# Performance work log

Hardware: AMD Instinct MI355X
Metric: run time of the kernel (lower is better)

The kernel has to match this reference:

```python
import jax, jax.numpy as jnp
import numpy as np

EPS = 1e-8


def setup_inputs() -> dict:
    key = jax.random.key(0)
    ks = jax.random.split(key, 7)
    B, H, S, D = 4, 16, 4096, 64
    query = jax.random.normal(ks[0], (B, H, S, D), dtype=jnp.float32)
    k_in = jax.random.normal(ks[1], (B, H, S, D), dtype=jnp.float32)
    value = jax.random.normal(ks[2], (B, H, S, D), dtype=jnp.float32)
    output = jax.random.normal(ks[3], (B, H, S, D), dtype=jnp.float32)
    betas = jax.random.normal(ks[4], (H, 1, D), dtype=jnp.float32)
    init_states = jax.random.normal(ks[5], (H, D, D), dtype=jnp.float32)
    init_z = jax.random.uniform(ks[6], (H, D), dtype=jnp.float32)
    return {"query": query, "key": k_in, "value": value, "output": output,
            "betas": betas, "init_states": init_states, "init_z": init_z}


def reference(query, key, value, output, betas, init_states, init_z):
    # ---- compute updates (delta rule) ----
    sigma_k = jax.nn.elu(key) + 1.0                       # [B,H,S,D]
    # retrieved_value = (sigma_k @ states) / (sigma_k @ z + eps)
    num = jnp.einsum('bhsd,hde->bhse', sigma_k, init_states)   # [B,H,S,D]
    den = jnp.einsum('bhsd,hd->bhs', sigma_k, init_z)[..., None] + EPS
    value_update = value - num / den                      # delta rule
    # memory_states = init_states + sigma_k^T @ value_update -> [B,H,D,D]
    memory_states = init_states[None] + jnp.einsum('bhsd,bhse->bhde', sigma_k, value_update)
    memory_z = init_z[None] + sigma_k.sum(axis=-2)        # [B,H,D]
    # ---- retrieve memory ----
    sigma_q = jax.nn.elu(query) + 1.0                     # [B,H,S,D]
    retrieved = jnp.einsum('bhsd,bhde->bhse', sigma_q, memory_states)
    norm = jnp.einsum('bhsd,bhd->bhs', sigma_q, memory_z)[..., None] + EPS
    memory_output = retrieved / norm                      # [B,H,S,D]
    # ---- sigmoid-gated blend ----
    gate = jax.nn.sigmoid(betas)                          # [H,1,D] broadcasts over B,S
    return gate * memory_output + (1.0 - gate) * output
```

## Files before the change

### kernel.cpp

```cpp
#include <hip/hip_runtime.h>
#include <hip/hip_bf16.h>


#define B_  4
#define H_  16
#define S_  4096
#define D_  64
#define BH_ 64
#define EPS_ 1e-8f

typedef __attribute__((ext_vector_type(8))) short bf16x8;
typedef __attribute__((ext_vector_type(4))) float f32x4;

__device__ __forceinline__ unsigned short f2bf(float x) {
    union { float f; unsigned u; } v; v.f = x;
    return (unsigned short)((v.u + 0x7FFFu + ((v.u >> 16) & 1u)) >> 16);
}
__device__ __forceinline__ float elup1(float x) {
    return x > 0.0f ? x + 1.0f : __expf(x);
}
__device__ __forceinline__ f32x4 fzero() { f32x4 z = {0.f, 0.f, 0.f, 0.f}; return z; }

__global__ __launch_bounds__(256, 2) void k1_states(
    const float* __restrict__ Kp, const float* __restrict__ Vp,
    const float* __restrict__ W0, const float* __restrict__ Z0,
    float* __restrict__ Mpart, float* __restrict__ Zpart, int NS)
{
    const int bh = blockIdx.x / NS;
    const int p  = blockIdx.x % NS;
    const int h  = bh & (H_ - 1);
    const int tid  = threadIdx.x;
    const int lane = tid & 63;
    const int wave = tid >> 6;
    const int c16  = lane & 15;
    const int g4   = lane >> 4;

    __shared__ __align__(16) unsigned short skT[4][64][40];
    __shared__ __align__(16) unsigned short vuT[4][64][40];
    __shared__ float Mlds[64 * 65];
    __shared__ float Zlds[4][64];

    float z0v[2][8];
    #pragma unroll
    for (int kk = 0; kk < 2; ++kk) {
        f32x4 a = *(const f32x4*)(Z0 + h * 64 + kk * 32 + g4 * 8);
        f32x4 b = *(const f32x4*)(Z0 + h * 64 + kk * 32 + g4 * 8 + 4);
        #pragma unroll
        for (int j = 0; j < 4; ++j) { z0v[kk][j] = a[j]; z0v[kk][4 + j] = b[j]; }
    }

    bf16x8 w0f[4][2];
    #pragma unroll
    for (int et = 0; et < 4; ++et)
    #pragma unroll
    for (int kk = 0; kk < 2; ++kk) {
        bf16x8 f;
        #pragma unroll
        for (int j = 0; j < 8; ++j) {
            int d = kk * 32 + g4 * 8 + j;
            f[j] = (short)f2bf(W0[(size_t)h * 4096 + d * 64 + et * 16 + c16]);
        }
        w0f[et][kk] = f;
    }

    const size_t baseKV  = (size_t)bh * S_ * D_;
    const int    schunk  = S_ / NS;
    const int    ngroups = schunk / 32;

    f32x4 mpa[4][4];
    #pragma unroll
    for (int i = 0; i < 4; ++i)
    #pragma unroll
    for (int j = 0; j < 4; ++j) mpa[i][j] = fzero();
    float zacc[2][8];
    #pragma unroll
    for (int kk = 0; kk < 2; ++kk)
    #pragma unroll
    for (int j = 0; j < 8; ++j) zacc[kk][j] = 0.f;

    for (int g = wave; g < ngroups; g += 4) {
        const int row0 = p * schunk + g * 32;

        float sk[2][2][8];
        #pragma unroll
        for (int st = 0; st < 2; ++st) {
            const float* kr = Kp + baseKV + (size_t)(row0 + st * 16 + c16) * D_;
            #pragma unroll
            for (int kk = 0; kk < 2; ++kk) {
                f32x4 a = *(const f32x4*)(kr + kk * 32 + g4 * 8);
                f32x4 b = *(const f32x4*)(kr + kk * 32 + g4 * 8 + 4);
                #pragma unroll
                for (int j = 0; j < 4; ++j) {
                    sk[st][kk][j]     = elup1(a[j]);
                    sk[st][kk][4 + j] = elup1(b[j]);
                }
            }
        }

        float den0 = 0.f, den1 = 0.f;
        #pragma unroll
        for (int kk = 0; kk < 2; ++kk)
        #pragma unroll
        for (int j = 0; j < 8; ++j) {
            den0 += sk[0][kk][j] * z0v[kk][j];
            den1 += sk[1][kk][j] * z0v[kk][j];
        }
        den0 += __shfl_xor(den0, 16); den0 += __shfl_xor(den0, 32);
        den1 += __shfl_xor(den1, 16); den1 += __shfl_xor(den1, 32);
        const float rd0 = __builtin_amdgcn_rcpf(den0 + EPS_);
        const float rd1 = __builtin_amdgcn_rcpf(den1 + EPS_);

        #pragma unroll
        for (int kk = 0; kk < 2; ++kk)
        #pragma unroll
        for (int j = 0; j < 8; ++j) zacc[kk][j] += sk[0][kk][j] + sk[1][kk][j];

        bf16x8 skf[2][2];
        #pragma unroll
        for (int kk = 0; kk < 2; ++kk)
        #pragma unroll
        for (int j = 0; j < 8; ++j) {
            unsigned short b0 = f2bf(sk[0][kk][j]);
            unsigned short b1 = f2bf(sk[1][kk][j]);
            skf[0][kk][j] = (short)b0;
            skf[1][kk][j] = (short)b1;
            *(unsigned*)&skT[wave][kk * 32 + g4 * 8 + j][2 * c16] =
                (unsigned)b0 | ((unsigned)b1 << 16);
        }

        f32x4 acc[2][4];
        #pragma unroll
        for (int st = 0; st < 2; ++st)
        #pragma unroll
        for (int et = 0; et < 4; ++et) {
            f32x4 t = __builtin_amdgcn_mfma_f32_16x16x32_bf16(w0f[et][0], skf[st][0], fzero(), 0, 0, 0);
            acc[st][et] = __builtin_amdgcn_mfma_f32_16x16x32_bf16(w0f[et][1], skf[st][1], t, 0, 0, 0);
        }

        const float* vr0 = Vp + baseKV + (size_t)(row0 + c16) * D_;
        const float* vr1 = Vp + baseKV + (size_t)(row0 + 16 + c16) * D_;
        #pragma unroll
        for (int et = 0; et < 4; ++et) {
            f32x4 v0 = *(const f32x4*)(vr0 + et * 16 + g4 * 4);
            f32x4 v1 = *(const f32x4*)(vr1 + et * 16 + g4 * 4);
            #pragma unroll
            for (int r = 0; r < 4; ++r) {
                float u0 = v0[r] - acc[0][et][r] * rd0;
                float u1 = v1[r] - acc[1][et][r] * rd1;
                *(unsigned*)&vuT[wave][et * 16 + g4 * 4 + r][2 * c16] =
                    (unsigned)f2bf(u0) | ((unsigned)f2bf(u1) << 16);
            }
        }

        bf16x8 am[4], bn[4];
        #pragma unroll
        for (int mt = 0; mt < 4; ++mt)
            am[mt] = *(const bf16x8*)&skT[wave][mt * 16 + c16][g4 * 8];
        #pragma unroll
        for (int nt = 0; nt < 4; ++nt)
            bn[nt] = *(const bf16x8*)&vuT[wave][nt * 16 + c16][g4 * 8];
        #pragma unroll
        for (int mt = 0; mt < 4; ++mt)
        #pragma unroll
        for (int nt = 0; nt < 4; ++nt)
            mpa[mt][nt] = __builtin_amdgcn_mfma_f32_16x16x32_bf16(am[mt], bn[nt], mpa[mt][nt], 0, 0, 0);
    }

    #pragma unroll
    for (int kk = 0; kk < 2; ++kk)
    #pragma unroll
    for (int j = 0; j < 8; ++j) {
        float z = zacc[kk][j];
        z += __shfl_xor(z, 1); z += __shfl_xor(z, 2);
        z += __shfl_xor(z, 4); z += __shfl_xor(z, 8);
        if (c16 == 0) Zlds[wave][kk * 32 + g4 * 8 + j] = z;
    }

    __syncthreads();
    for (int w = 0; w < 4; ++w) {
        if (wave == w) {
            #pragma unroll
            for (int mt = 0; mt < 4; ++mt)
            #pragma unroll
            for (int nt = 0; nt < 4; ++nt)
            #pragma unroll
            for (int r = 0; r < 4; ++r) {
                int idx = (mt * 16 + g4 * 4 + r) * 65 + nt * 16 + c16;
                float v = mpa[mt][nt][r];
                Mlds[idx] = (w == 0) ? v : (Mlds[idx] + v);
            }
        }
        __syncthreads();
    }

    float* mout = Mpart + ((size_t)p * BH_ + bh) * 4096;
    #pragma unroll
    for (int i = 0; i < 16; ++i) {
        int idx = i * 256 + tid;
        mout[idx] = Mlds[(idx >> 6) * 65 + (idx & 63)];
    }
    if (tid < 64) {
        float zs = Zlds[0][tid] + Zlds[1][tid] + Zlds[2][tid] + Zlds[3][tid];
        Zpart[((size_t)p * BH_ + bh) * 64 + tid] = zs;
    }
}

__global__ void k_reduce(const float* __restrict__ Mpart, const float* __restrict__ Zpart,
                         const float* __restrict__ W0, const float* __restrict__ Z0,
                         float* __restrict__ Mfin, float* __restrict__ Zfin, int NS)
{
    const int bh = blockIdx.x, h = bh & (H_ - 1), t = threadIdx.x;
    #pragma unroll
    for (int i = 0; i < 4; ++i) {
        int fi = i * 256 + t;
        f32x4 s = *(const f32x4*)(W0 + (size_t)h * 4096 + fi * 4);
        for (int p = 0; p < NS; ++p) {
            f32x4 v = *(const f32x4*)(Mpart + ((size_t)p * BH_ + bh) * 4096 + fi * 4);
            s = s + v;
        }
        *(f32x4*)(Mfin + (size_t)bh * 4096 + fi * 4) = s;
    }
    if (t < 64) {
        float s = Z0[h * 64 + t];
        for (int p = 0; p < NS; ++p) s += Zpart[((size_t)p * BH_ + bh) * 64 + t];
        Zfin[bh * 64 + t] = s;
    }
}

__global__ __launch_bounds__(256, 2) void k2_out(
    const float* __restrict__ Qp, const float* __restrict__ Op,
    const float* __restrict__ Bp, const float* __restrict__ Mfin,
    const float* __restrict__ Zfin, float* __restrict__ Out, int NS2)
{
    const int bh = blockIdx.x / NS2;
    const int p  = blockIdx.x % NS2;
    const int h  = bh & (H_ - 1);
    const int tid = threadIdx.x, lane = tid & 63, wave = tid >> 6;
    const int c16 = lane & 15, g4 = lane >> 4;

    float mzv[2][8];
    #pragma unroll
    for (int kk = 0; kk < 2; ++kk) {
        f32x4 a = *(const f32x4*)(Zfin + bh * 64 + kk * 32 + g4 * 8);
        f32x4 b = *(const f32x4*)(Zfin + bh * 64 + kk * 32 + g4 * 8 + 4);
        #pragma unroll
        for (int j = 0; j < 4; ++j) { mzv[kk][j] = a[j]; mzv[kk][4 + j] = b[j]; }
    }

    bf16x8 mf[4][2];
    #pragma unroll
    for (int et = 0; et < 4; ++et)
    #pragma unroll
    for (int kk = 0; kk < 2; ++kk) {
        bf16x8 f;
        #pragma unroll
        for (int j = 0; j < 8; ++j)
            f[j] = (short)f2bf(Mfin[(size_t)bh * 4096 + (kk * 32 + g4 * 8 + j) * 64 + et * 16 + c16]);
        mf[et][kk] = f;
    }

    float gate[4][4];
    #pragma unroll
    for (int et = 0; et < 4; ++et)
    #pragma unroll
    for (int r = 0; r < 4; ++r) {
        float b = Bp[h * 64 + et * 16 + g4 * 4 + r];
        gate[et][r] = 1.0f / (1.0f + __expf(-b));
    }

    const size_t base = (size_t)bh * S_ * D_;
    const int schunk = S_ / NS2, ngroups = schunk / 32;

    for (int g = wave; g < ngroups; g += 4) {
        const int row0 = p * schunk + g * 32;

        float sq[2][2][8];
        #pragma unroll
        for (int st = 0; st < 2; ++st) {
            const float* qr = Qp + base + (size_t)(row0 + st * 16 + c16) * D_;
            #pragma unroll
            for (int kk = 0; kk < 2; ++kk) {
                f32x4 a = *(const f32x4*)(qr + kk * 32 + g4 * 8);
                f32x4 b = *(const f32x4*)(qr + kk * 32 + g4 * 8 + 4);
                #pragma unroll
                for (int j = 0; j < 4; ++j) {
                    sq[st][kk][j]     = elup1(a[j]);
                    sq[st][kk][4 + j] = elup1(b[j]);
                }
            }
        }

        float n0 = 0.f, n1 = 0.f;
        #pragma unroll
        for (int kk = 0; kk < 2; ++kk)
        #pragma unroll
        for (int j = 0; j < 8; ++j) {
            n0 += sq[0][kk][j] * mzv[kk][j];
            n1 += sq[1][kk][j] * mzv[kk][j];
        }
        n0 += __shfl_xor(n0, 16); n0 += __shfl_xor(n0, 32);
        n1 += __shfl_xor(n1, 16); n1 += __shfl_xor(n1, 32);
        const float rn0 = __builtin_amdgcn_rcpf(n0 + EPS_);
        const float rn1 = __builtin_amdgcn_rcpf(n1 + EPS_);

        bf16x8 sqf[2][2];
        #pragma unroll
        for (int st = 0; st < 2; ++st)
        #pragma unroll
        for (int kk = 0; kk < 2; ++kk) {
            bf16x8 f;
            #pragma unroll
            for (int j = 0; j < 8; ++j) f[j] = (short)f2bf(sq[st][kk][j]);
            sqf[st][kk] = f;
        }

        f32x4 acc[2][4];
        #pragma unroll
        for (int st = 0; st < 2; ++st)
        #pragma unroll
        for (int et = 0; et < 4; ++et) {
            f32x4 t = __builtin_amdgcn_mfma_f32_16x16x32_bf16(mf[et][0], sqf[st][0], fzero(), 0, 0, 0);
            acc[st][et] = __builtin_amdgcn_mfma_f32_16x16x32_bf16(mf[et][1], sqf[st][1], t, 0, 0, 0);
        }

        #pragma unroll
        for (int st = 0; st < 2; ++st) {
            const float rn = st ? rn1 : rn0;
            const size_t roff = base + (size_t)(row0 + st * 16 + c16) * D_;
            #pragma unroll
            for (int et = 0; et < 4; ++et) {
                f32x4 o4 = *(const f32x4*)(Op + roff + et * 16 + g4 * 4);
                f32x4 w;
                #pragma unroll
                for (int r = 0; r < 4; ++r) {
                    float t = acc[st][et][r] * rn;
                    w[r] = o4[r] + gate[et][r] * (t - o4[r]);
                }
                *(f32x4*)(Out + roff + et * 16 + g4 * 4) = w;
            }
        }
    }
}

extern "C" void kernel_launch(void* const* d_in, const int* in_sizes, int n_in,
                              void* d_out, int out_size, void* d_ws, size_t ws_size,
                              hipStream_t stream)
{
    const float* Q  = (const float*)d_in[0];
    const float* K  = (const float*)d_in[1];
    const float* V  = (const float*)d_in[2];
    const float* O  = (const float*)d_in[3];
    const float* Bt = (const float*)d_in[4];
    const float* W0 = (const float*)d_in[5];
    const float* Z0 = (const float*)d_in[6];
    float* Out = (float*)d_out;

    int NS = 8;
    auto need = [](int ns) -> size_t {
        return sizeof(float) * ((size_t)ns * BH_ * 4096 + (size_t)ns * BH_ * 64 +
                                (size_t)BH_ * 4096 + (size_t)BH_ * 64);
    };
    while (NS > 1 && need(NS) > ws_size) NS >>= 1;

    float* Mpart = (float*)d_ws;
    float* Zpart = Mpart + (size_t)NS * BH_ * 4096;
    float* Mfin  = Zpart + (size_t)NS * BH_ * 64;
    float* Zfin  = Mfin + (size_t)BH_ * 4096;

    hipLaunchKernelGGL(k1_states, dim3(BH_ * NS), dim3(256), 0, stream,
                       K, V, W0, Z0, Mpart, Zpart, NS);
    hipLaunchKernelGGL(k_reduce, dim3(BH_), dim3(256), 0, stream,
                       Mpart, Zpart, W0, Z0, Mfin, Zfin, NS);
    hipLaunchKernelGGL(k2_out, dim3(BH_ * 8), dim3(256), 0, stream,
                       Q, O, Bt, Mfin, Zfin, Out, 8);
}
```

Baseline: 99.78 us.

## Pre-transpose states to bf16, union LDS buffers, raise split and occupancy

Adds a prep kernel that transposes and converts W0 to bf16 once, and makes the reduce kernel emit the final memory state transposed in bf16. The k1 and k2 fragment loads then become single vector loads instead of strided scalar gathers with per-element conversion. k1 overlays its staging and reduction LDS arrays in a union, and launch bounds rise to 4 blocks per CU. The sequence split grows from 8 to 16 chunks in both passes and the reduce grid widens. The cost is an extra kernel launch and a larger partial-state buffer for the reduce pass to read.

```diff
diff --git a/kernel.cpp b/kernel.cpp
--- a/kernel.cpp
+++ b/kernel.cpp
@@ -11,6 +11,7 @@
 
 typedef __attribute__((ext_vector_type(8))) short bf16x8;
 typedef __attribute__((ext_vector_type(4))) float f32x4;
+typedef __attribute__((ext_vector_type(4))) unsigned short u16x4;
 
 __device__ __forceinline__ unsigned short f2bf(float x) {
     union { float f; unsigned u; } v; v.f = x;
@@ -21,9 +22,20 @@
 }
 __device__ __forceinline__ f32x4 fzero() { f32x4 z = {0.f, 0.f, 0.f, 0.f}; return z; }
 
-__global__ __launch_bounds__(256, 2) void k1_states(
+__global__ void k0_prep(const float* __restrict__ W0, unsigned short* __restrict__ W0T)
+{
+    const int h = blockIdx.x, t = threadIdx.x;
+    #pragma unroll
+    for (int i = 0; i < 16; ++i) {
+        int o = i * 256 + t;
+        int e = o >> 6, d = o & 63;
+        W0T[h * 4096 + o] = f2bf(W0[(size_t)h * 4096 + d * 64 + e]);
+    }
+}
+
+__global__ __launch_bounds__(256, 4) void k1_states(
     const float* __restrict__ Kp, const float* __restrict__ Vp,
-    const float* __restrict__ W0, const float* __restrict__ Z0,
+    const unsigned short* __restrict__ W0T, const float* __restrict__ Z0,
     float* __restrict__ Mpart, float* __restrict__ Zpart, int NS)
 {
     const int bh = blockIdx.x / NS;
@@ -35,10 +47,10 @@
     const int c16  = lane & 15;
     const int g4   = lane >> 4;
 
-    __shared__ __align__(16) unsigned short skT[4][64][40];
-    __shared__ __align__(16) unsigned short vuT[4][64][40];
-    __shared__ float Mlds[64 * 65];
-    __shared__ float Zlds[4][64];
+    __shared__ __align__(16) union {
+        struct { unsigned short skT[4][64][40], vuT[4][64][40]; } a;
+        struct { float M[64 * 65]; float Z[4][64]; } b;
+    } U;
 
     float z0v[2][8];
     #pragma unroll
@@ -53,15 +65,8 @@
     #pragma unroll
     for (int et = 0; et < 4; ++et)
     #pragma unroll
-    for (int kk = 0; kk < 2; ++kk) {
-        bf16x8 f;
-        #pragma unroll
-        for (int j = 0; j < 8; ++j) {
-            int d = kk * 32 + g4 * 8 + j;
-            f[j] = (short)f2bf(W0[(size_t)h * 4096 + d * 64 + et * 16 + c16]);
-        }
-        w0f[et][kk] = f;
-    }
+    for (int kk = 0; kk < 2; ++kk)
+        w0f[et][kk] = *(const bf16x8*)(W0T + h * 4096 + (et * 16 + c16) * 64 + kk * 32 + g4 * 8);
 
     const size_t baseKV  = (size_t)bh * S_ * D_;
     const int    schunk  = S_ / NS;
@@ -124,7 +129,7 @@
             unsigned short b1 = f2bf(sk[1][kk][j]);
             skf[0][kk][j] = (short)b0;
             skf[1][kk][j] = (short)b1;
-            *(unsigned*)&skT[wave][kk * 32 + g4 * 8 + j][2 * c16] =
+            *(unsigned*)&U.a.skT[wave][kk * 32 + g4 * 8 + j][2 * c16] =
                 (unsigned)b0 | ((unsigned)b1 << 16);
         }
 
@@ -147,7 +152,7 @@
             for (int r = 0; r < 4; ++r) {
                 float u0 = v0[r] - acc[0][et][r] * rd0;
                 float u1 = v1[r] - acc[1][et][r] * rd1;
-                *(unsigned*)&vuT[wave][et * 16 + g4 * 4 + r][2 * c16] =
+                *(unsigned*)&U.a.vuT[wave][et * 16 + g4 * 4 + r][2 * c16] =
                     (unsigned)f2bf(u0) | ((unsigned)f2bf(u1) << 16);
             }
         }
@@ -155,16 +160,18 @@
         bf16x8 am[4], bn[4];
         #pragma unroll
         for (int mt = 0; mt < 4; ++mt)
-            am[mt] = *(const bf16x8*)&skT[wave][mt * 16 + c16][g4 * 8];
+            am[mt] = *(const bf16x8*)&U.a.skT[wave][mt * 16 + c16][g4 * 8];
         #pragma unroll
         for (int nt = 0; nt < 4; ++nt)
-            bn[nt] = *(const bf16x8*)&vuT[wave][nt * 16 + c16][g4 * 8];
+            bn[nt] = *(const bf16x8*)&U.a.vuT[wave][nt * 16 + c16][g4 * 8];
         #pragma unroll
         for (int mt = 0; mt < 4; ++mt)
         #pragma unroll
         for (int nt = 0; nt < 4; ++nt)
             mpa[mt][nt] = __builtin_amdgcn_mfma_f32_16x16x32_bf16(am[mt], bn[nt], mpa[mt][nt], 0, 0, 0);
     }
+
+    __syncthreads();
 
     #pragma unroll
     for (int kk = 0; kk < 2; ++kk)
@@ -173,10 +180,9 @@
         float z = zacc[kk][j];
         z += __shfl_xor(z, 1); z += __shfl_xor(z, 2);
         z += __shfl_xor(z, 4); z += __shfl_xor(z, 8);
-        if (c16 == 0) Zlds[wave][kk * 32 + g4 * 8 + j] = z;
-    }
-
-    __syncthreads();
+        if (c16 == 0) U.b.Z[wave][kk * 32 + g4 * 8 + j] = z;
+    }
+
     for (int w = 0; w < 4; ++w) {
         if (wave == w) {
             #pragma unroll
@@ -187,7 +193,7 @@
             for (int r = 0; r < 4; ++r) {
                 int idx = (mt * 16 + g4 * 4 + r) * 65 + nt * 16 + c16;
                 float v = mpa[mt][nt][r];
-                Mlds[idx] = (w == 0) ? v : (Mlds[idx] + v);
+                U.b.M[idx] = (w == 0) ? v : (U.b.M[idx] + v);
             }
         }
         __syncthreads();
@@ -197,39 +203,47 @@
     #pragma unroll
     for (int i = 0; i < 16; ++i) {
         int idx = i * 256 + tid;
-        mout[idx] = Mlds[(idx >> 6) * 65 + (idx & 63)];
+        mout[idx] = U.b.M[(idx >> 6) * 65 + (idx & 63)];
     }
     if (tid < 64) {
-        float zs = Zlds[0][tid] + Zlds[1][tid] + Zlds[2][tid] + Zlds[3][tid];
+        float zs = U.b.Z[0][tid] + U.b.Z[1][tid] + U.b.Z[2][tid] + U.b.Z[3][tid];
         Zpart[((size_t)p * BH_ + bh) * 64 + tid] = zs;
     }
 }
 
 __global__ void k_reduce(const float* __restrict__ Mpart, const float* __restrict__ Zpart,
                          const float* __restrict__ W0, const float* __restrict__ Z0,
-                         float* __restrict__ Mfin, float* __restrict__ Zfin, int NS)
-{
-    const int bh = blockIdx.x, h = bh & (H_ - 1), t = threadIdx.x;
-    #pragma unroll
-    for (int i = 0; i < 4; ++i) {
-        int fi = i * 256 + t;
-        f32x4 s = *(const f32x4*)(W0 + (size_t)h * 4096 + fi * 4);
-        for (int p = 0; p < NS; ++p) {
-            f32x4 v = *(const f32x4*)(Mpart + ((size_t)p * BH_ + bh) * 4096 + fi * 4);
-            s = s + v;
-        }
-        *(f32x4*)(Mfin + (size_t)bh * 4096 + fi * 4) = s;
-    }
-    if (t < 64) {
-        float s = Z0[h * 64 + t];
-        for (int p = 0; p < NS; ++p) s += Zpart[((size_t)p * BH_ + bh) * 64 + t];
-        Zfin[bh * 64 + t] = s;
-    }
-}
-
-__global__ __launch_bounds__(256, 2) void k2_out(
+                         unsigned short* __restrict__ MfinT, float* __restrict__ Zfin, int NS)
+{
+    const int bh = blockIdx.x >> 2, q = blockIdx.x & 3;
+    const int h = bh & (H_ - 1), t = threadIdx.x;
+    __shared__ float Ml[16][65];
+
+    const int o = q * 1024 + t * 4;
+    f32x4 s = *(const f32x4*)(W0 + (size_t)h * 4096 + o);
+    for (int p = 0; p < NS; ++p)
+        s = s + *(const f32x4*)(Mpart + ((size_t)p * BH_ + bh) * 4096 + o);
+    const int dl = t >> 4, e0 = (t & 15) * 4;
+    #pragma unroll
+    for (int j = 0; j < 4; ++j) Ml[dl][e0 + j] = s[j];
+    __syncthreads();
+
+    const int e = t >> 2, dd0 = (t & 3) * 4;
+    u16x4 w;
+    #pragma unroll
+    for (int j = 0; j < 4; ++j) w[j] = f2bf(Ml[dd0 + j][e]);
+    *(u16x4*)(MfinT + (size_t)bh * 4096 + e * 64 + q * 16 + dd0) = w;
+
+    if (q == 0 && t < 64) {
+        float zs = Z0[h * 64 + t];
+        for (int p = 0; p < NS; ++p) zs += Zpart[((size_t)p * BH_ + bh) * 64 + t];
+        Zfin[bh * 64 + t] = zs;
+    }
+}
+
+__global__ __launch_bounds__(256, 4) void k2_out(
     const float* __restrict__ Qp, const float* __restrict__ Op,
-    const float* __restrict__ Bp, const float* __restrict__ Mfin,
+    const float* __restrict__ Bp, const unsigned short* __restrict__ MfinT,
     const float* __restrict__ Zfin, float* __restrict__ Out, int NS2)
 {
     const int bh = blockIdx.x / NS2;
@@ -251,13 +265,8 @@
     #pragma unroll
     for (int et = 0; et < 4; ++et)
     #pragma unroll
-    for (int kk = 0; kk < 2; ++kk) {
-        bf16x8 f;
-        #pragma unroll
-        for (int j = 0; j < 8; ++j)
-            f[j] = (short)f2bf(Mfin[(size_t)bh * 4096 + (kk * 32 + g4 * 8 + j) * 64 + et * 16 + c16]);
-        mf[et][kk] = f;
-    }
+    for (int kk = 0; kk < 2; ++kk)
+        mf[et][kk] = *(const bf16x8*)(MfinT + (size_t)bh * 4096 + (et * 16 + c16) * 64 + kk * 32 + g4 * 8);
 
     float gate[4][4];
     #pragma unroll
@@ -355,22 +364,24 @@
     const float* Z0 = (const float*)d_in[6];
     float* Out = (float*)d_out;
 
-    int NS = 8;
+    int NS = 16;
     auto need = [](int ns) -> size_t {
-        return sizeof(float) * ((size_t)ns * BH_ * 4096 + (size_t)ns * BH_ * 64 +
-                                (size_t)BH_ * 4096 + (size_t)BH_ * 64);
+        return sizeof(float) * ((size_t)ns * BH_ * 4096 + (size_t)ns * BH_ * 64 + BH_ * 64) +
+               sizeof(unsigned short) * ((size_t)BH_ * 4096 + (size_t)H_ * 4096);
     };
     while (NS > 1 && need(NS) > ws_size) NS >>= 1;
 
     float* Mpart = (float*)d_ws;
     float* Zpart = Mpart + (size_t)NS * BH_ * 4096;
-    float* Mfin  = Zpart + (size_t)NS * BH_ * 64;
-    float* Zfin  = Mfin + (size_t)BH_ * 4096;
-
+    float* Zfin  = Zpart + (size_t)NS * BH_ * 64;
+    unsigned short* MfinT = (unsigned short*)(Zfin + (size_t)BH_ * 64);
+    unsigned short* W0T   = MfinT + (size_t)BH_ * 4096;
+
+    hipLaunchKernelGGL(k0_prep, dim3(H_), dim3(256), 0, stream, W0, W0T);
     hipLaunchKernelGGL(k1_states, dim3(BH_ * NS), dim3(256), 0, stream,
-                       K, V, W0, Z0, Mpart, Zpart, NS);
-    hipLaunchKernelGGL(k_reduce, dim3(BH_), dim3(256), 0, stream,
-                       Mpart, Zpart, W0, Z0, Mfin, Zfin, NS);
-    hipLaunchKernelGGL(k2_out, dim3(BH_ * 8), dim3(256), 0, stream,
-                       Q, O, Bt, Mfin, Zfin, Out, 8);
-}
+                       K, V, W0T, Z0, Mpart, Zpart, NS);
+    hipLaunchKernelGGL(k_reduce, dim3(BH_ * 4), dim3(256), 0, stream,
+                       Mpart, Zpart, W0, Z0, MfinT, Zfin, NS);
+    hipLaunchKernelGGL(k2_out, dim3(BH_ * 16), dim3(256), 0, stream,
+                       Q, O, Bt, MfinT, Zfin, Out, 16);
+}
```

After: 160.4 us. 60.7% more time.
